# Kernel optimization log

Measured on AMD Instinct MI355X. Metric: run time of the kernel, lower is better.

The kernel has to match this reference:

```python
import jax, jax.numpy as jnp
import numpy as np

BETA = 0.5

def setup_inputs() -> dict:
    key = jax.random.key(0)
    ks = jax.random.split(key, 10)
    B, H = 4096, 200
    ITEM, REGION = 100000, 1000
    D, HID = 128, 64  # embed_size, hidden_size
    half = D // 2
    history = jax.random.randint(ks[0], (B, H), 0, ITEM)
    target = jax.random.randint(ks[1], (B,), 0, ITEM)
    history_region = jax.random.randint(ks[2], (B, H), 0, REGION)
    target_region = jax.random.randint(ks[3], (B,), 0, REGION)
    W_hist = jax.random.normal(ks[4], (ITEM, half), jnp.float32) * 0.01
    W_tgt = jax.random.normal(ks[5], (ITEM, half), jnp.float32) * 0.01
    W_reg = jax.random.normal(ks[6], (REGION, half), jnp.float32) * 0.01
    W1 = jax.random.normal(ks[7], (D, HID), jnp.float32) * (1.0 / np.sqrt(D))
    b1 = jnp.zeros((HID,), jnp.float32)
    W2 = jax.random.normal(ks[8], (HID,), jnp.float32) * (1.0 / np.sqrt(HID))
    return {"history": history, "target": target,
            "history_region": history_region, "target_region": target_region,
            "W_hist": W_hist, "W_tgt": W_tgt, "W_reg": W_reg,
            "W1": W1, "b1": b1, "W2": W2}

def reference(history, target, history_region, target_region,
              W_hist, W_tgt, W_reg, W1, b1, W2):
    # gather + concat: [B,H,D] and [B,D]
    h = jnp.concatenate([W_hist[history], W_reg[history_region]], axis=-1)
    t = jnp.concatenate([W_tgt[target], W_reg[target_region]], axis=-1)
    inp = h * t[:, None, :]                      # [B,H,D]
    r1 = jax.nn.relu(inp @ W1 + b1)              # [B,H,HID] (dropout = identity at eval)
    logits = r1 @ W2                             # [B,H]
    mask = (history != target[:, None]).astype(logits.dtype)
    exp_A = jnp.exp(logits) * mask               # [B,H]
    exp_sum = jnp.sum(exp_A, axis=-1) ** BETA    # [B], beta-power normalization
    attn = exp_A / exp_sum[:, None]              # [B,H]
    pred = jnp.einsum('bhd,bd->b', h * attn[..., None], t)
    return jax.nn.sigmoid(pred)
```

## Files before the change

kernel.cpp:

```cpp
#include <hip/hip_runtime.h>
#include <math.h>

#define NB        4096
#define NH        200
#define HIST_ROWS 100000
#define REG_ROWS  1000
#define NTILES    13

typedef __attribute__((ext_vector_type(4))) int   int4i;

#define SA 2048.0f
#define SB 16384.0f
#define ST 2048.0f
#define INV_LOGIT (1.0f / (SA * SB))
#define INV_S     (1.0f / (SA * ST))

__device__ __forceinline__ int q8(float x, float s) {
    return __float2int_rn(fminf(fmaxf(x * s, -127.f), 127.f));
}
__device__ __forceinline__ int pack4(float a, float b, float c, float d, float s) {
    const int x0 = q8(a, s), x1 = q8(b, s), x2 = q8(c, s), x3 = q8(d, s);
    return (x0 & 255) | ((x1 & 255) << 8) | ((x2 & 255) << 16) | (x3 << 24);
}

__global__ __launch_bounds__(256) void prep_i8(
    const float* __restrict__ Wh, const float* __restrict__ Wr,
    const float* __restrict__ W1,
    unsigned char* __restrict__ tab, float* __restrict__ W1F2)
{
    for (int i = blockIdx.x * blockDim.x + threadIdx.x; i < 10240;
         i += gridDim.x * blockDim.x) {
        const int chunk = i >> 4, j = i & 15;
        const int frag = chunk >> 6, nt = frag >> 1, ks = frag & 1;
        const int c = chunk & 63, q = c >> 4, l = c & 15;
        W1F2[i] = (nt < 4) ? W1[(ks * 64 + q * 16 + j) * 64 + nt * 16 + l] : 0.f;
    }
    const int total = (HIST_ROWS + REG_ROWS) * 16;
    const int HE    = HIST_ROWS * 16;
    unsigned* dst = (unsigned*)tab;
    for (int i = blockIdx.x * blockDim.x + threadIdx.x; i < total;
         i += gridDim.x * blockDim.x) {
        const float4 v = (i < HE) ? ((const float4*)Wh)[i]
                                  : ((const float4*)Wr)[i - HE];
        dst[i] = (unsigned)pack4(v.x, v.y, v.z, v.w, SA);
    }
}

__global__ __launch_bounds__(64, 3) void nais_w64(
    const int*   __restrict__ history,
    const int*   __restrict__ target,
    const int*   __restrict__ history_region,
    const int*   __restrict__ target_region,
    const float* __restrict__ W_tgt,
    const float* __restrict__ W_reg,
    const float* __restrict__ b1,
    const float* __restrict__ W2,
    const unsigned char* __restrict__ tab,
    const float* __restrict__ W1F2,
    float*       __restrict__ out)
{
    const int lane = threadIdx.x & 63;
    const int b    = blockIdx.x;
    const int l15  = lane & 15, quad = lane >> 4;
    const int r_sel = l15 & 3;
    const int bNH  = b * NH;
    const int q16  = quad * 16;

    const int tgt  = target[b];
    const int treg = target_region[b];
    const float* tW = W_tgt + (size_t)tgt * 64;
    const float* rW = W_reg + (size_t)treg * 64;

    int4i sAh0, sAr0, sAh1, sAr1, sAh2, sAr2;
    int   mIh0, mIr0, mIh1, mIr1, mIh2, mIr2;

#define LOADIDX(S, T) do {                                                    \
        int j_ = (T) * 16 + l15;                                              \
        if (j_ >= NH) j_ = NH - 1;             \
        mIh##S = history[bNH + j_];                                           \
        mIr##S = history_region[bNH + j_];                                    \
    } while (0)

#define GATH(S) do {                                                          \
        sAh##S = *(const int4i*)(tab + (size_t)mIh##S * 64 + q16);            \
        sAr##S = *(const int4i*)(tab + (size_t)(HIST_ROWS + mIr##S) * 64 + q16); \
    } while (0)

    LOADIDX(0, 0); GATH(0);
    LOADIDX(1, 1); GATH(1);
    LOADIDX(2, 2); GATH(2);

    int4i bf0, bf1, bf2, bf3, bf4, bf5, bf6, bf7, bf8, bf9;
#define BFB(V) do {                                                           \
        const float4* tp_ = (const float4*)((((V) & 1) ? rW : tW) + q16);     \
        const float4 t0_ = tp_[0], t1_ = tp_[1], t2_ = tp_[2], t3_ = tp_[3];  \
        if ((V) < 8) {                                                        \
            const float4* wp_ = (const float4*)(W1F2 + ((V) * 64 + lane) * 16); \
            const float4 w0_ = wp_[0], w1_ = wp_[1], w2_ = wp_[2], w3_ = wp_[3]; \
            bf##V.x = pack4(w0_.x * t0_.x, w0_.y * t0_.y, w0_.z * t0_.z, w0_.w * t0_.w, SB); \
            bf##V.y = pack4(w1_.x * t1_.x, w1_.y * t1_.y, w1_.z * t1_.z, w1_.w * t1_.w, SB); \
            bf##V.z = pack4(w2_.x * t2_.x, w2_.y * t2_.y, w2_.z * t2_.z, w2_.w * t2_.w, SB); \
            bf##V.w = pack4(w3_.x * t3_.x, w3_.y * t3_.y, w3_.z * t3_.z, w3_.w * t3_.w, SB); \
        } else {                           \
            if (l15 == 0) {                                                   \
                bf##V.x = pack4(t0_.x, t0_.y, t0_.z, t0_.w, ST);              \
                bf##V.y = pack4(t1_.x, t1_.y, t1_.z, t1_.w, ST);              \
                bf##V.z = pack4(t2_.x, t2_.y, t2_.z, t2_.w, ST);              \
                bf##V.w = pack4(t3_.x, t3_.y, t3_.z, t3_.w, ST);              \
            } else {                                                          \
                bf##V = (int4i){0, 0, 0, 0};                                  \
            }                                                                 \
        }                                                                     \
    } while (0)
    BFB(0); BFB(1); BFB(2); BFB(3); BFB(4);
    BFB(5); BFB(6); BFB(7); BFB(8); BFB(9);
#undef BFB

    const float w2_0 = W2[l15],      w2_1 = W2[16 + l15];
    const float w2_2 = W2[32 + l15], w2_3 = W2[48 + l15];
    const float b1_0 = b1[l15],      b1_1 = b1[16 + l15];
    const float b1_2 = b1[32 + l15], b1_3 = b1[48 + l15];

    float e_acc = 0.f, p_acc = 0.f;

#define EPINT(NT) do {                                                        \
        p0_ += fmaxf((float)acc##NT[0] * INV_LOGIT + b1_##NT, 0.f) * w2_##NT; \
        p1_ += fmaxf((float)acc##NT[1] * INV_LOGIT + b1_##NT, 0.f) * w2_##NT; \
        p2_ += fmaxf((float)acc##NT[2] * INV_LOGIT + b1_##NT, 0.f) * w2_##NT; \
        p3_ += fmaxf((float)acc##NT[3] * INV_LOGIT + b1_##NT, 0.f) * w2_##NT; \
    } while (0)
#define XR(P) do {                                                            \
        P += __shfl_xor(P, 1); P += __shfl_xor(P, 2);                         \
        P += __shfl_xor(P, 4); P += __shfl_xor(P, 8);                         \
    } while (0)

#define BODY(S, T) do {                                                       \
        int4i acc0 = {0,0,0,0}, acc1 = {0,0,0,0}, acc2 = {0,0,0,0};           \
        int4i acc3 = {0,0,0,0}, acc4 = {0,0,0,0};                             \
        acc0 = __builtin_amdgcn_mfma_i32_16x16x64_i8(sAh##S, bf0, acc0, 0, 0, 0); \
        acc1 = __builtin_amdgcn_mfma_i32_16x16x64_i8(sAh##S, bf2, acc1, 0, 0, 0); \
        acc2 = __builtin_amdgcn_mfma_i32_16x16x64_i8(sAh##S, bf4, acc2, 0, 0, 0); \
        acc3 = __builtin_amdgcn_mfma_i32_16x16x64_i8(sAh##S, bf6, acc3, 0, 0, 0); \
        acc4 = __builtin_amdgcn_mfma_i32_16x16x64_i8(sAh##S, bf8, acc4, 0, 0, 0); \
        acc0 = __builtin_amdgcn_mfma_i32_16x16x64_i8(sAr##S, bf1, acc0, 0, 0, 0); \
        acc1 = __builtin_amdgcn_mfma_i32_16x16x64_i8(sAr##S, bf3, acc1, 0, 0, 0); \
        acc2 = __builtin_amdgcn_mfma_i32_16x16x64_i8(sAr##S, bf5, acc2, 0, 0, 0); \
        acc3 = __builtin_amdgcn_mfma_i32_16x16x64_i8(sAr##S, bf7, acc3, 0, 0, 0); \
        acc4 = __builtin_amdgcn_mfma_i32_16x16x64_i8(sAr##S, bf9, acc4, 0, 0, 0); \
        float p0_ = 0.f, p1_ = 0.f, p2_ = 0.f, p3_ = 0.f;                     \
        EPINT(0); EPINT(1); EPINT(2); EPINT(3);                               \
        XR(p0_); XR(p1_); XR(p2_); XR(p3_);                                   \
        const float lgA_ = (r_sel & 1) ? p1_ : p0_;                           \
        const float lgB_ = (r_sel & 1) ? p3_ : p2_;                           \
        const float lg_  = (r_sel & 2) ? lgB_ : lgA_;                         \
        const float sv0_ = (float)__shfl(acc4[0], lane & 48);                 \
        const float sv1_ = (float)__shfl(acc4[1], lane & 48);                 \
        const float sv2_ = (float)__shfl(acc4[2], lane & 48);                 \
        const float sv3_ = (float)__shfl(acc4[3], lane & 48);                 \
        const float svA_ = (r_sel & 1) ? sv1_ : sv0_;                         \
        const float svB_ = (r_sel & 1) ? sv3_ : sv2_;                         \
        const float s_own_ = ((r_sel & 2) ? svB_ : svA_) * INV_S;             \
        const int  ihj_  = __shfl(mIh##S, quad * 4 + r_sel);                  \
        const int  jrow_ = (T) * 16 + quad * 4 + r_sel;                       \
        const bool valid_ = (l15 < 4) && (jrow_ < NH) && (ihj_ != tgt);       \
        const float ex_ = valid_ ? expf(lg_) : 0.f;                          \
        e_acc += ex_;                                                         \
        p_acc += ex_ * s_own_;                                                \
    } while (0)

    BODY(0, 0);   LOADIDX(0, 3);  GATH(0);
    BODY(1, 1);   LOADIDX(1, 4);  GATH(1);
    BODY(2, 2);   LOADIDX(2, 5);  GATH(2);
    BODY(0, 3);   LOADIDX(0, 6);  GATH(0);
    BODY(1, 4);   LOADIDX(1, 7);  GATH(1);
    BODY(2, 5);   LOADIDX(2, 8);  GATH(2);
    BODY(0, 6);   LOADIDX(0, 9);  GATH(0);
    BODY(1, 7);   LOADIDX(1, 10); GATH(1);
    BODY(2, 8);   LOADIDX(2, 11); GATH(2);
    BODY(0, 9);   LOADIDX(0, 12); GATH(0);
    BODY(1, 10);
    BODY(2, 11);
    BODY(0, 12);
#undef BODY
#undef EPINT
#undef XR
#undef GATH
#undef LOADIDX

    #pragma unroll
    for (int off = 1; off < 64; off <<= 1) {
        e_acc += __shfl_xor(e_acc, off);
        p_acc += __shfl_xor(p_acc, off);
    }
    if (lane == 0) {
        const float pred = p_acc / sqrtf(e_acc);
        out[b] = 1.f / (1.f + expf(-pred));
    }
}

__device__ __forceinline__ void epi_store_i8(
    const int4i* accT, const float* w2v, const float* b1v,
    int tl, int quad, int l15, float* logit_lds, float* s_lds)
{
    float part[4] = {0.f, 0.f, 0.f, 0.f};
    #pragma unroll
    for (int nt = 0; nt < 4; ++nt)
        #pragma unroll
        for (int r = 0; r < 4; ++r)
            part[r] += fmaxf((float)accT[nt][r] * INV_LOGIT + b1v[nt], 0.f) * w2v[nt];
    #pragma unroll
    for (int r = 0; r < 4; ++r) {
        part[r] += __shfl_xor(part[r], 1);
        part[r] += __shfl_xor(part[r], 2);
        part[r] += __shfl_xor(part[r], 4);
        part[r] += __shfl_xor(part[r], 8);
    }
    if (l15 == 0) {
        const int jg = tl * 16 + quad * 4;
        #pragma unroll
        for (int r = 0; r < 4; ++r) {
            logit_lds[jg + r] = part[r];
            s_lds[jg + r]     = (float)accT[4][r] * INV_S;
        }
    }
}

__device__ __forceinline__ int4i quant_row_fp32(const float* row, int quad) {
    const float4* p = (const float4*)(row + quad * 16);
    const float4 v0 = p[0], v1 = p[1], v2 = p[2], v3 = p[3];
    int4i o;
    o.x = pack4(v0.x, v0.y, v0.z, v0.w, SA);
    o.y = pack4(v1.x, v1.y, v1.z, v1.w, SA);
    o.z = pack4(v2.x, v2.y, v2.z, v2.w, SA);
    o.w = pack4(v3.x, v3.y, v3.z, v3.w, SA);
    return o;
}

__global__ __launch_bounds__(256, 3) void nais_fb(
    const int*   __restrict__ history,
    const int*   __restrict__ target,
    const int*   __restrict__ history_region,
    const int*   __restrict__ target_region,
    const float* __restrict__ W_hist,
    const float* __restrict__ W_tgt,
    const float* __restrict__ W_reg,
    const float* __restrict__ W1,
    const float* __restrict__ b1,
    const float* __restrict__ W2,
    float*       __restrict__ out)
{
    __shared__ int hist_lds[224];
    __shared__ int hreg_lds[224];
    __shared__ __align__(16) float t_lds[128];
    __shared__ __align__(16) int Bf4[640 * 4];
    __shared__ float logit_lds[208];
    __shared__ float s_lds[208];
    __shared__ float red_e[4], red_p[4];

    const int b   = blockIdx.x;
    const int tid = threadIdx.x;
    const int tgt = target[b];

    if (tid < 224) {
        const int jj = tid < NH ? tid : NH - 1;
        hist_lds[tid] = history[b * NH + jj];
        hreg_lds[tid] = history_region[b * NH + jj];
    }
    if (tid < 64) {
        t_lds[tid] = W_tgt[(size_t)tgt * 64 + tid];
    } else if (tid < 128) {
        t_lds[tid] = W_reg[(size_t)target_region[b] * 64 + (tid - 64)];
    }
    __syncthreads();

    const int lane = tid & 63, wv = tid >> 6;
    const int l15  = lane & 15, quad = lane >> 4;
    const int  tls[4] = {wv, wv + 4, wv + 8, wv + 12};
    const bool has3   = (tls[3] < NTILES);

    #pragma unroll
    for (int v = 0; v < 3; ++v) {
        const int i = tid + v * 256;
        if (i < 640) {
            const int frag = i >> 6, nt = frag >> 1, ks = frag & 1;
            const int c = i & 63, q = c >> 4, l = c & 15;
            const int k0 = ks * 64 + q * 16;
            const float4 t0 = *(const float4*)(t_lds + k0);
            const float4 t1 = *(const float4*)(t_lds + k0 + 4);
            const float4 t2 = *(const float4*)(t_lds + k0 + 8);
            const float4 t3 = *(const float4*)(t_lds + k0 + 12);
            int4i ob;
            if (nt < 4) {
                const int n = nt * 16 + l;
                float tmp[16];
                #pragma unroll
                for (int j = 0; j < 16; ++j) tmp[j] = W1[(k0 + j) * 64 + n];
                ob.x = pack4(tmp[0] * t0.x, tmp[1] * t0.y, tmp[2] * t0.z, tmp[3] * t0.w, SB);
                ob.y = pack4(tmp[4] * t1.x, tmp[5] * t1.y, tmp[6] * t1.z, tmp[7] * t1.w, SB);
                ob.z = pack4(tmp[8] * t2.x, tmp[9] * t2.y, tmp[10] * t2.z, tmp[11] * t2.w, SB);
                ob.w = pack4(tmp[12] * t3.x, tmp[13] * t3.y, tmp[14] * t3.z, tmp[15] * t3.w, SB);
            } else {
                if (l == 0) {
                    ob.x = pack4(t0.x, t0.y, t0.z, t0.w, ST);
                    ob.y = pack4(t1.x, t1.y, t1.z, t1.w, ST);
                    ob.z = pack4(t2.x, t2.y, t2.z, t2.w, ST);
                    ob.w = pack4(t3.x, t3.y, t3.z, t3.w, ST);
                } else {
                    ob = (int4i){0, 0, 0, 0};
                }
            }
            *reinterpret_cast<int4i*>(&Bf4[i * 4]) = ob;
        }
    }
    __syncthreads();

    float w2v[4], b1v[4];
    #pragma unroll
    for (int nt = 0; nt < 4; ++nt) {
        w2v[nt] = W2[nt * 16 + l15];
        b1v[nt] = b1[nt * 16 + l15];
    }

    int4i A[4][2];
    #pragma unroll
    for (int pp = 0; pp < 2; ++pp) {
        const int t0i = pp * 2, t1i = pp * 2 + 1;
        const bool hb = (t1i < 3) || has3;

        #pragma unroll
        for (int tt = 0; tt < 2; ++tt) {
            const int ti = t0i + tt;
            const int j  = ((ti == 3 && !has3) ? tls[2] : tls[ti]) * 16 + l15;
            A[ti][0] = quant_row_fp32(W_hist + (size_t)hist_lds[j] * 64, quad);
            A[ti][1] = quant_row_fp32(W_reg  + (size_t)hreg_lds[j] * 64, quad);
        }

        int4i acc[2][5];
        #pragma unroll
        for (int tt = 0; tt < 2; ++tt)
            #pragma unroll
            for (int nt = 0; nt < 5; ++nt) acc[tt][nt] = (int4i){0, 0, 0, 0};

        #pragma unroll
        for (int ks = 0; ks < 2; ++ks) {
            int4i bfr[5];
            #pragma unroll
            for (int nt = 0; nt < 5; ++nt)
                bfr[nt] = *reinterpret_cast<const int4i*>(&Bf4[((nt * 2 + ks) * 64 + lane) * 4]);
            #pragma unroll
            for (int nt = 0; nt < 5; ++nt)
                acc[0][nt] = __builtin_amdgcn_mfma_i32_16x16x64_i8(A[t0i][ks], bfr[nt], acc[0][nt], 0, 0, 0);
            if (hb) {
                #pragma unroll
                for (int nt = 0; nt < 5; ++nt)
                    acc[1][nt] = __builtin_amdgcn_mfma_i32_16x16x64_i8(A[t1i][ks], bfr[nt], acc[1][nt], 0, 0, 0);
            }
        }

        epi_store_i8(acc[0], w2v, b1v, tls[t0i], quad, l15, logit_lds, s_lds);
        if (hb) epi_store_i8(acc[1], w2v, b1v, tls[t1i], quad, l15, logit_lds, s_lds);
    }
    __syncthreads();

    float e = 0.f, p = 0.f;
    if (tid < NH) {
        const float ex = (hist_lds[tid] != tgt) ? expf(logit_lds[tid]) : 0.f;
        e = ex;
        p = ex * s_lds[tid];
    }
    #pragma unroll
    for (int off = 32; off > 0; off >>= 1) {
        e += __shfl_down(e, off);
        p += __shfl_down(p, off);
    }
    if (lane == 0) { red_e[wv] = e; red_p[wv] = p; }
    __syncthreads();
    if (tid == 0) {
        const float E = red_e[0] + red_e[1] + red_e[2] + red_e[3];
        const float P = red_p[0] + red_p[1] + red_p[2] + red_p[3];
        const float pred = P / sqrtf(E);
        out[b] = 1.f / (1.f + expf(-pred));
    }
}

extern "C" void kernel_launch(void* const* d_in, const int* in_sizes, int n_in,
                              void* d_out, int out_size, void* d_ws, size_t ws_size,
                              hipStream_t stream) {
    const int*   history        = (const int*)  d_in[0];
    const int*   target         = (const int*)  d_in[1];
    const int*   history_region = (const int*)  d_in[2];
    const int*   target_region  = (const int*)  d_in[3];
    const float* W_hist         = (const float*)d_in[4];
    const float* W_tgt          = (const float*)d_in[5];
    const float* W_reg          = (const float*)d_in[6];
    const float* W1             = (const float*)d_in[7];
    const float* b1             = (const float*)d_in[8];
    const float* W2             = (const float*)d_in[9];
    float* out = (float*)d_out;

    const size_t tab_bytes = (size_t)(HIST_ROWS + REG_ROWS) * 64;
    const size_t need = tab_bytes + 10240 * 4;
    if (ws_size >= need) {
        unsigned char* tab = (unsigned char*)d_ws;
        float* W1F2 = (float*)((char*)d_ws + tab_bytes);
        prep_i8<<<2048, 256, 0, stream>>>(W_hist, W_reg, W1, tab, W1F2);
        nais_w64<<<NB, 64, 0, stream>>>(history, target, history_region, target_region,
                                        W_tgt, W_reg, b1, W2, tab, W1F2, out);
    } else {
        nais_fb<<<NB, 256, 0, stream>>>(history, target, history_region, target_region,
                                        W_hist, W_tgt, W_reg, W1, b1, W2, out);
    }
}
```

Baseline: 151.9 us.

## Pack four batch rows per block and keep per-row B fragments in LDS

Launches 256-thread blocks with one wavefront per batch row instead of 64-thread blocks. The ten per-row MFMA B fragments now sit in shared memory and are reloaded from LDS each iteration instead of living in 40 VGPRs. The aim is to cut register pressure so more waves stay resident and gather latency is hidden better. The cost is extra LDS reads per tile and a block-wide barrier.

```diff
diff --git a/kernel.cpp b/kernel.cpp
--- a/kernel.cpp
+++ b/kernel.cpp
@@ -46,7 +46,7 @@
     }
 }
 
-__global__ __launch_bounds__(64, 3) void nais_w64(
+__global__ __launch_bounds__(256, 3) void nais_wl(
     const int*   __restrict__ history,
     const int*   __restrict__ target,
     const int*   __restrict__ history_region,
@@ -59,8 +59,11 @@
     const float* __restrict__ W1F2,
     float*       __restrict__ out)
 {
-    const int lane = threadIdx.x & 63;
-    const int b    = blockIdx.x;
+    __shared__ __align__(16) int Bw[4 * 640 * 4];
+
+    const int tid  = threadIdx.x;
+    const int lane = tid & 63, wv = tid >> 6;
+    const int b    = blockIdx.x * 4 + wv;
     const int l15  = lane & 15, quad = lane >> 4;
     const int r_sel = l15 & 3;
     const int bNH  = b * NH;
@@ -70,6 +73,9 @@
     const int treg = target_region[b];
     const float* tW = W_tgt + (size_t)tgt * 64;
     const float* rW = W_reg + (size_t)treg * 64;
+
+    int4i*       Bst = (int4i*)Bw + wv * 640;
+    const int4i* Bp  = (const int4i*)Bw + wv * 640;
 
     int4i sAh0, sAr0, sAh1, sAr1, sAh2, sAr2;
     int   mIh0, mIr0, mIh1, mIr1, mIh2, mIr2;
@@ -90,31 +96,32 @@
     LOADIDX(1, 1); GATH(1);
     LOADIDX(2, 2); GATH(2);
 
-    int4i bf0, bf1, bf2, bf3, bf4, bf5, bf6, bf7, bf8, bf9;
-#define BFB(V) do {                                                           \
-        const float4* tp_ = (const float4*)((((V) & 1) ? rW : tW) + q16);     \
-        const float4 t0_ = tp_[0], t1_ = tp_[1], t2_ = tp_[2], t3_ = tp_[3];  \
-        if ((V) < 8) {                                                        \
-            const float4* wp_ = (const float4*)(W1F2 + ((V) * 64 + lane) * 16); \
-            const float4 w0_ = wp_[0], w1_ = wp_[1], w2_ = wp_[2], w3_ = wp_[3]; \
-            bf##V.x = pack4(w0_.x * t0_.x, w0_.y * t0_.y, w0_.z * t0_.z, w0_.w * t0_.w, SB); \
-            bf##V.y = pack4(w1_.x * t1_.x, w1_.y * t1_.y, w1_.z * t1_.z, w1_.w * t1_.w, SB); \
-            bf##V.z = pack4(w2_.x * t2_.x, w2_.y * t2_.y, w2_.z * t2_.z, w2_.w * t2_.w, SB); \
-            bf##V.w = pack4(w3_.x * t3_.x, w3_.y * t3_.y, w3_.z * t3_.z, w3_.w * t3_.w, SB); \
-        } else {                           \
-            if (l15 == 0) {                                                   \
-                bf##V.x = pack4(t0_.x, t0_.y, t0_.z, t0_.w, ST);              \
-                bf##V.y = pack4(t1_.x, t1_.y, t1_.z, t1_.w, ST);              \
-                bf##V.z = pack4(t2_.x, t2_.y, t2_.z, t2_.w, ST);              \
-                bf##V.w = pack4(t3_.x, t3_.y, t3_.z, t3_.w, ST);              \
-            } else {                                                          \
-                bf##V = (int4i){0, 0, 0, 0};                                  \
-            }                                                                 \
-        }                                                                     \
-    } while (0)
-    BFB(0); BFB(1); BFB(2); BFB(3); BFB(4);
-    BFB(5); BFB(6); BFB(7); BFB(8); BFB(9);
-#undef BFB
+    #pragma unroll
+    for (int v = 0; v < 10; ++v) {
+        const int ks = v & 1;
+        const float4* tp = (const float4*)((ks ? rW : tW) + q16);
+        const float4 t0 = tp[0], t1 = tp[1], t2 = tp[2], t3 = tp[3];
+        int4i ob;
+        if (v < 8) {
+            const float4* wp = (const float4*)(W1F2 + (v * 64 + lane) * 16);
+            const float4 w0 = wp[0], w1 = wp[1], w2 = wp[2], w3 = wp[3];
+            ob.x = pack4(w0.x * t0.x, w0.y * t0.y, w0.z * t0.z, w0.w * t0.w, SB);
+            ob.y = pack4(w1.x * t1.x, w1.y * t1.y, w1.z * t1.z, w1.w * t1.w, SB);
+            ob.z = pack4(w2.x * t2.x, w2.y * t2.y, w2.z * t2.z, w2.w * t2.w, SB);
+            ob.w = pack4(w3.x * t3.x, w3.y * t3.y, w3.z * t3.z, w3.w * t3.w, SB);
+        } else {
+            if (l15 == 0) {
+                ob.x = pack4(t0.x, t0.y, t0.z, t0.w, ST);
+                ob.y = pack4(t1.x, t1.y, t1.z, t1.w, ST);
+                ob.z = pack4(t2.x, t2.y, t2.z, t2.w, ST);
+                ob.w = pack4(t3.x, t3.y, t3.z, t3.w, ST);
+            } else {
+                ob = (int4i){0, 0, 0, 0};
+            }
+        }
+        Bst[v * 64 + lane] = ob;
+    }
+    __syncthreads();
 
     const float w2_0 = W2[l15],      w2_1 = W2[16 + l15];
     const float w2_2 = W2[32 + l15], w2_3 = W2[48 + l15];
@@ -135,18 +142,24 @@
     } while (0)
 
 #define BODY(S, T) do {                                                       \
+        asm volatile("" ::: "memory");                                        \
+        const int4i bq0 = Bp[0 * 64 + lane], bq1 = Bp[1 * 64 + lane];         \
+        const int4i bq2 = Bp[2 * 64 + lane], bq3 = Bp[3 * 64 + lane];         \
+        const int4i bq4 = Bp[4 * 64 + lane], bq5 = Bp[5 * 64 + lane];         \
+        const int4i bq6 = Bp[6 * 64 + lane], bq7 = Bp[7 * 64 + lane];         \
+        const int4i bq8 = Bp[8 * 64 + lane], bq9 = Bp[9 * 64 + lane];         \
         int4i acc0 = {0,0,0,0}, acc1 = {0,0,0,0}, acc2 = {0,0,0,0};           \
         int4i acc3 = {0,0,0,0}, acc4 = {0,0,0,0};                             \
-        acc0 = __builtin_amdgcn_mfma_i32_16x16x64_i8(sAh##S, bf0, acc0, 0, 0, 0); \
-        acc1 = __builtin_amdgcn_mfma_i32_16x16x64_i8(sAh##S, bf2, acc1, 0, 0, 0); \
-        acc2 = __builtin_amdgcn_mfma_i32_16x16x64_i8(sAh##S, bf4, acc2, 0, 0, 0); \
-        acc3 = __builtin_amdgcn_mfma_i32_16x16x64_i8(sAh##S, bf6, acc3, 0, 0, 0); \
-        acc4 = __builtin_amdgcn_mfma_i32_16x16x64_i8(sAh##S, bf8, acc4, 0, 0, 0); \
-        acc0 = __builtin_amdgcn_mfma_i32_16x16x64_i8(sAr##S, bf1, acc0, 0, 0, 0); \
-        acc1 = __builtin_amdgcn_mfma_i32_16x16x64_i8(sAr##S, bf3, acc1, 0, 0, 0); \
-        acc2 = __builtin_amdgcn_mfma_i32_16x16x64_i8(sAr##S, bf5, acc2, 0, 0, 0); \
-        acc3 = __builtin_amdgcn_mfma_i32_16x16x64_i8(sAr##S, bf7, acc3, 0, 0, 0); \
-        acc4 = __builtin_amdgcn_mfma_i32_16x16x64_i8(sAr##S, bf9, acc4, 0, 0, 0); \
+        acc0 = __builtin_amdgcn_mfma_i32_16x16x64_i8(sAh##S, bq0, acc0, 0, 0, 0); \
+        acc1 = __builtin_amdgcn_mfma_i32_16x16x64_i8(sAh##S, bq2, acc1, 0, 0, 0); \
+        acc2 = __builtin_amdgcn_mfma_i32_16x16x64_i8(sAh##S, bq4, acc2, 0, 0, 0); \
+        acc3 = __builtin_amdgcn_mfma_i32_16x16x64_i8(sAh##S, bq6, acc3, 0, 0, 0); \
+        acc4 = __builtin_amdgcn_mfma_i32_16x16x64_i8(sAh##S, bq8, acc4, 0, 0, 0); \
+        acc0 = __builtin_amdgcn_mfma_i32_16x16x64_i8(sAr##S, bq1, acc0, 0, 0, 0); \
+        acc1 = __builtin_amdgcn_mfma_i32_16x16x64_i8(sAr##S, bq3, acc1, 0, 0, 0); \
+        acc2 = __builtin_amdgcn_mfma_i32_16x16x64_i8(sAr##S, bq5, acc2, 0, 0, 0); \
+        acc3 = __builtin_amdgcn_mfma_i32_16x16x64_i8(sAr##S, bq7, acc3, 0, 0, 0); \
+        acc4 = __builtin_amdgcn_mfma_i32_16x16x64_i8(sAr##S, bq9, acc4, 0, 0, 0); \
         float p0_ = 0.f, p1_ = 0.f, p2_ = 0.f, p3_ = 0.f;                     \
         EPINT(0); EPINT(1); EPINT(2); EPINT(3);                               \
         XR(p0_); XR(p1_); XR(p2_); XR(p3_);                                   \
@@ -404,8 +417,8 @@
         unsigned char* tab = (unsigned char*)d_ws;
         float* W1F2 = (float*)((char*)d_ws + tab_bytes);
         prep_i8<<<2048, 256, 0, stream>>>(W_hist, W_reg, W1, tab, W1F2);
-        nais_w64<<<NB, 64, 0, stream>>>(history, target, history_region, target_region,
-                                        W_tgt, W_reg, b1, W2, tab, W1F2, out);
+        nais_wl<<<NB / 4, 256, 0, stream>>>(history, target, history_region, target_region,
+                                            W_tgt, W_reg, b1, W2, tab, W1F2, out);
     } else {
         nais_fb<<<NB, 256, 0, stream>>>(history, target, history_region, target_region,
                                         W_hist, W_tgt, W_reg, W1, b1, W2, out);
```

Measured after the change: 142.4 us. -6.3%, faster.
